# Optimization experiments

Hardware: AMD Instinct MI355X
Metric: run time of the kernel (lower is better)

The kernel has to match this reference:

```python
import jax, jax.numpy as jnp
import numpy as np

BETA = 0.25

def setup_inputs() -> dict:
    key = jax.random.key(0)
    k1, k2 = jax.random.split(key)
    x = jax.random.normal(k1, (16, 256, 32, 32), dtype=jnp.float32)
    emb_weight = jax.random.normal(k2, (8192, 256), dtype=jnp.float32) * 0.02
    return {"x": x, "emb_weight": emb_weight}

def reference(x, emb_weight):
    # b c h w -> b h w c
    xt = jnp.transpose(x, (0, 2, 3, 1))
    D = emb_weight.shape[1]
    xf = xt.reshape(-1, D)  # [N, D]
    # squared euclidean distances: [N, K]
    dist = (jnp.sum(xf * xf, axis=1, keepdims=True)
            + jnp.sum(emb_weight * emb_weight, axis=1)
            - 2.0 * xf @ emb_weight.T)
    indices = jnp.argmin(dist, axis=1)  # [N]
    x_q = emb_weight[indices].reshape(xt.shape)  # [B,H,W,D]
    sg = jax.lax.stop_gradient
    loss = (BETA * jnp.mean(jnp.square(sg(x_q) - xt))
            + jnp.mean(jnp.square(x_q - sg(xt))))
    # straight-through estimator
    x_q_st = xt + sg(x_q - xt)
    out = jnp.transpose(x_q_st, (0, 3, 1, 2))  # b h w c -> b c h w
    return out, loss, indices
```

## Files before the change

kernel.cpp:

```cpp
#include <hip/hip_runtime.h>

#define NPTS   16384
#define KCODES 8192
#define DDIM   256
#define HWSZ   1024
#define CHW    (DDIM * HWSZ)
#define OUT_ELEMS 4194304
#define LOSS_OFF  OUT_ELEMS
#define IDX_OFF   (OUT_ELEMS + 1)

#define PTB   64
#define CTILE 128
#define KC    64
#define NIT   256
#define XPITCH 264

#define ARENA_B 133120
#define XH_OFF  65536
#define XL_OFF  99328

typedef _Float16 half_t;
typedef __attribute__((ext_vector_type(8))) _Float16 half8;
typedef __attribute__((ext_vector_type(4))) float     v4f;

union HU { _Float16 h; unsigned short u; };

#define EHI_WORDS  (256 * 8192)
#define SE_OFF_B   (2 * EHI_WORDS * 2)

#define GLD16(gp, lp) __builtin_amdgcn_global_load_lds( \
    (const __attribute__((address_space(1))) unsigned int*)(gp), \
    (__attribute__((address_space(3))) unsigned int*)(lp), 16, 0, 0)

__global__ void prep_kernel(const float* __restrict__ emb,
                            unsigned short* __restrict__ ehi,
                            unsigned short* __restrict__ elo,
                            float* __restrict__ se)
{
    const int gw   = (blockIdx.x * 256 + threadIdx.x) >> 6;
    const int lane = threadIdx.x & 63;
    for (int i = 0; i < 8; ++i) {
        const int c = gw * 8 + i;
        const float4 v = *(const float4*)(emb + (size_t)c * DDIM + lane * 4);
        float ps = v.x * v.x;
        ps = fmaf(v.y, v.y, ps); ps = fmaf(v.z, v.z, ps); ps = fmaf(v.w, v.w, ps);
        float tot = ps;
        #pragma unroll
        for (int off = 1; off < 64; off <<= 1) tot += __shfl_xor(tot, off);
        if (lane == 0) se[c] = tot;
        const float E0 = v.x * 64.f, E1 = v.y * 64.f, E2 = v.z * 64.f, E3 = v.w * 64.f;
        const half_t h0 = (half_t)E0, h1 = (half_t)E1, h2 = (half_t)E2, h3 = (half_t)E3;
        const half_t l0 = (half_t)((E0 - (float)h0) * 2048.f);
        const half_t l1 = (half_t)((E1 - (float)h1) * 2048.f);
        const half_t l2 = (half_t)((E2 - (float)h2) * 2048.f);
        const half_t l3 = (half_t)((E3 - (float)h3) * 2048.f);
        HU a0, a1, a2, a3, b0, b1, b2, b3;
        a0.h = h0; a1.h = h1; a2.h = h2; a3.h = h3;
        b0.h = l0; b1.h = l1; b2.h = l2; b3.h = l3;
        const unsigned int uh0 = (unsigned)a0.u | ((unsigned)a1.u << 16);
        const unsigned int uh1 = (unsigned)a2.u | ((unsigned)a3.u << 16);
        const unsigned int ul0 = (unsigned)b0.u | ((unsigned)b1.u << 16);
        const unsigned int ul1 = (unsigned)b2.u | ((unsigned)b3.u << 16);
        const int ck = lane >> 4;
        const int kb = (lane & 15) >> 1;
        const int hf = lane & 1;
        const int T = c >> 7, r = c & 127;
        const size_t base = (((size_t)(T * 4 + ck) * 128 + r) * 64)
                          + (size_t)((kb ^ (r & 7)) * 8) + hf * 4;
        *(unsigned int*)&ehi[base]     = uh0;
        *(unsigned int*)&ehi[base + 2] = uh1;
        *(unsigned int*)&elo[base]     = ul0;
        *(unsigned int*)&elo[base + 2] = ul1;
    }
}

__launch_bounds__(512)
__global__ void vq_kernel(const float* __restrict__ x,
                          const unsigned short* __restrict__ ehi,
                          const unsigned short* __restrict__ elo,
                          const float* __restrict__ wse,
                          const float* __restrict__ emb,
                          float* __restrict__ out)
{
    __shared__ __align__(16) char ldsA[ARENA_B];
    __shared__ float  ldsRS[8][65];
    __shared__ float  ldsS[PTB];
    __shared__ float  ldsFD[8][32];
    __shared__ int    ldsFI[8][32];
    __shared__ int    ldsI[PTB];
    __shared__ double ldsL[8];

    const int t    = threadIdx.x;
    const int lane = t & 63;
    const int w    = t >> 6;
    const int n0   = blockIdx.x * PTB;
    const int b    = n0 / HWSZ;
    const int hw0  = n0 % HWSZ;
    const float* xs = x + (size_t)b * CHW + hw0;

    unsigned short* XHp = (unsigned short*)(ldsA + XH_OFF);
    unsigned short* XLp = (unsigned short*)(ldsA + XL_OFF);

    const int part = (w & 3) * 4096;
    #define STAGE(img, q) do { \
        const char* _g = (const char*)((w < 4) ? ehi : elo) \
                       + (size_t)(img) * 16384 + part + lane * 16; \
        char* _l = ldsA + (size_t)(q) * 32768 + ((w < 4) ? 0 : 16384) + part; \
        GLD16(_g,          _l); \
        GLD16(_g + 1024,   _l + 1024); \
        GLD16(_g + 2048,   _l + 2048); \
        GLD16(_g + 3072,   _l + 3072); \
    } while (0)

    STAGE(0, 0);
    STAGE(1, 1);

    {
        const int p   = t & 63;
        const int seg = t >> 6;
        float a = 0.f;
        for (int i = 0; i < 32; ++i) {
            const int c = seg * 32 + i;
            const float v = xs[(size_t)c * HWSZ + p];
            const half_t hh = (half_t)v;
            const half_t hl = (half_t)((v - (float)hh) * 2048.0f);
            HU u0; u0.h = hh; XHp[p * XPITCH + c] = u0.u;
            HU u1; u1.h = hl; XLp[p * XPITCH + c] = u1.u;
            a = fmaf(v, v, a);
        }
        ldsRS[seg][p] = a;
    }
    __syncthreads();
    if (t < PTB) {
        float s = 0.f;
        for (int g = 0; g < 8; ++g) s += ldsRS[g][t];
        ldsS[t] = s;
    }
    __syncthreads();

    const int h32 = (w & 1) * 32;
    const int q32 = (w >> 1) * 32;
    const int ln  = lane & 15;
    const int qd  = lane >> 4;

    float s_frag[8];
    #pragma unroll
    for (int pbi = 0; pbi < 2; ++pbi)
        #pragma unroll
        for (int r = 0; r < 4; ++r)
            s_frag[pbi * 4 + r] = ldsS[h32 + pbi * 16 + qd * 4 + r];

    half8 aH[2][4][2], aL[2][4][2];
    #pragma unroll
    for (int pb = 0; pb < 2; ++pb)
        #pragma unroll
        for (int ck = 0; ck < 4; ++ck)
            #pragma unroll
            for (int kk = 0; kk < 2; ++kk) {
                const int ka = ck * KC + kk * 32 + qd * 8;
                aH[pb][ck][kk] = *(const half8*)&XHp[(h32 + pb * 16 + ln) * XPITCH + ka];
                aL[pb][ck][kk] = *(const half8*)&XLp[(h32 + pb * 16 + ln) * XPITCH + ka];
            }
    asm volatile("s_waitcnt lgkmcnt(0)" ::: "memory");
    __syncthreads();

    float best_d[8]; int best_i[8];
    #pragma unroll
    for (int i = 0; i < 8; ++i) { best_d[i] = 3.4e38f; best_i[i] = 0; }

    v4f acc_hh[2][2], acc_hl[2][2];
    float se0 = 0.f, se1 = 0.f;

    const int rL = (q32 + ln) * 64;
    const int rH = (q32 + 16 + ln) * 64;

    #define CHUNK(CK) do { \
        const unsigned short* EHp = (const unsigned short*)(ldsA + (CK) * 32768); \
        const unsigned short* ELp = (const unsigned short*)(ldsA + (CK) * 32768 + 16384); \
        _Pragma("unroll") \
        for (int kk = 0; kk < 2; ++kk) { \
            const int swz = ((kk * 4 + qd) ^ (ln & 7)) * 8; \
            const half8 bh0 = *(const half8*)&EHp[rL + swz]; \
            const half8 bh1 = *(const half8*)&EHp[rH + swz]; \
            const half8 bl0 = *(const half8*)&ELp[rL + swz]; \
            const half8 bl1 = *(const half8*)&ELp[rH + swz]; \
            acc_hh[0][0] = __builtin_amdgcn_mfma_f32_16x16x32_f16(aH[0][CK][kk], bh0, acc_hh[0][0], 0, 0, 0); \
            acc_hh[0][1] = __builtin_amdgcn_mfma_f32_16x16x32_f16(aH[0][CK][kk], bh1, acc_hh[0][1], 0, 0, 0); \
            acc_hh[1][0] = __builtin_amdgcn_mfma_f32_16x16x32_f16(aH[1][CK][kk], bh0, acc_hh[1][0], 0, 0, 0); \
            acc_hh[1][1] = __builtin_amdgcn_mfma_f32_16x16x32_f16(aH[1][CK][kk], bh1, acc_hh[1][1], 0, 0, 0); \
            acc_hl[0][0] = __builtin_amdgcn_mfma_f32_16x16x32_f16(aH[0][CK][kk], bl0, acc_hl[0][0], 0, 0, 0); \
            acc_hl[0][1] = __builtin_amdgcn_mfma_f32_16x16x32_f16(aH[0][CK][kk], bl1, acc_hl[0][1], 0, 0, 0); \
            acc_hl[1][0] = __builtin_amdgcn_mfma_f32_16x16x32_f16(aH[1][CK][kk], bl0, acc_hl[1][0], 0, 0, 0); \
            acc_hl[1][1] = __builtin_amdgcn_mfma_f32_16x16x32_f16(aH[1][CK][kk], bl1, acc_hl[1][1], 0, 0, 0); \
            acc_hl[0][0] = __builtin_amdgcn_mfma_f32_16x16x32_f16(aL[0][CK][kk], bh0, acc_hl[0][0], 0, 0, 0); \
            acc_hl[0][1] = __builtin_amdgcn_mfma_f32_16x16x32_f16(aL[0][CK][kk], bh1, acc_hl[0][1], 0, 0, 0); \
            acc_hl[1][0] = __builtin_amdgcn_mfma_f32_16x16x32_f16(aL[1][CK][kk], bh0, acc_hl[1][0], 0, 0, 0); \
            acc_hl[1][1] = __builtin_amdgcn_mfma_f32_16x16x32_f16(aL[1][CK][kk], bh1, acc_hl[1][1], 0, 0, 0); \
        } \
    } while (0)

    for (int tile = 0; tile < 64; ++tile) {
        const int it0 = tile * 4;
        __builtin_amdgcn_s_barrier();
        STAGE(it0 + 2, 2);
        STAGE(it0 + 3, 3);
        asm volatile("s_waitcnt vmcnt(8)" ::: "memory");
        __builtin_amdgcn_s_barrier();
        __builtin_amdgcn_s_setprio(1);
        #pragma unroll
        for (int i = 0; i < 2; ++i)
            #pragma unroll
            for (int j = 0; j < 2; ++j)
                #pragma unroll
                for (int r = 0; r < 4; ++r) { acc_hh[i][j][r] = 0.f; acc_hl[i][j][r] = 0.f; }
        CHUNK(0);
        CHUNK(1);
        __builtin_amdgcn_s_setprio(0);
        {
            const int tb2 = tile * CTILE;
            se0 = wse[tb2 + q32 + ln];
            se1 = wse[tb2 + q32 + 16 + ln];
        }
        __builtin_amdgcn_s_barrier();
        if (tile + 1 < 64) {
            STAGE(it0 + 4, 0);
            STAGE(it0 + 5, 1);
            asm volatile("s_waitcnt vmcnt(8)" ::: "memory");
        } else {
            asm volatile("s_waitcnt vmcnt(0)" ::: "memory");
        }
        __builtin_amdgcn_s_barrier();
        __builtin_amdgcn_s_setprio(1);
        CHUNK(2);
        CHUNK(3);
        __builtin_amdgcn_s_setprio(0);
        {
            const int tb = tile * CTILE;
            #pragma unroll
            for (int csi = 0; csi < 2; ++csi) {
                const float se   = csi ? se1 : se0;
                const int   code = tb + q32 + csi * 16 + ln;
                #pragma unroll
                for (int pbi = 0; pbi < 2; ++pbi)
                    #pragma unroll
                    for (int r = 0; r < 4; ++r) {
                        const float m  = fmaf(acc_hl[pbi][csi][r], 4.8828125e-4f,
                                              acc_hh[pbi][csi][r]) * 0.015625f;
                        const float T  = s_frag[pbi * 4 + r] + se;
                        const float dd = fmaf(-2.0f, m, T);
                        const int   s  = pbi * 4 + r;
                        if (dd < best_d[s]) { best_d[s] = dd; best_i[s] = code; }
                    }
            }
        }
    }

    #pragma unroll
    for (int off = 1; off < 16; off <<= 1) {
        #pragma unroll
        for (int s = 0; s < 8; ++s) {
            const float d2 = __shfl_xor(best_d[s], off);
            const int   i2 = __shfl_xor(best_i[s], off);
            if (d2 < best_d[s] || (d2 == best_d[s] && i2 < best_i[s])) {
                best_d[s] = d2; best_i[s] = i2;
            }
        }
    }
    if (ln == 0) {
        #pragma unroll
        for (int pbi = 0; pbi < 2; ++pbi)
            #pragma unroll
            for (int r = 0; r < 4; ++r) {
                ldsFD[w][pbi * 16 + qd * 4 + r] = best_d[pbi * 4 + r];
                ldsFI[w][pbi * 16 + qd * 4 + r] = best_i[pbi * 4 + r];
            }
    }
    __syncthreads();
    if (t < PTB) {
        const int hh  = t >> 5;
        const int r32 = t & 31;
        float bd = 3.4e38f; int bi = 0;
        #pragma unroll
        for (int qq = 0; qq < 4; ++qq) {
            const int wv = hh + qq * 2;
            const float d2 = ldsFD[wv][r32];
            const int   i2 = ldsFI[wv][r32];
            if (d2 < bd || (d2 == bd && i2 < bi)) { bd = d2; bi = i2; }
        }
        ldsI[t] = bi;
        out[(size_t)IDX_OFF + n0 + t] = (float)bi;
    }
    __syncthreads();

    double lsum = 0.0;
    {
        const int p  = t & 63;
        const int cg = t >> 6;
        const int row = ldsI[p];
        const float* erow = emb + (size_t)row * DDIM;
        float* ob = out + (size_t)b * CHW + hw0 + p;
        for (int q = 0; q < 32; ++q) {
            const int c = cg * 32 + q;
            const float e  = erow[c];
            const float xx = xs[(size_t)c * HWSZ + p];
            const float diff = e - xx;
            ob[(size_t)c * HWSZ] = xx + diff;
            lsum += (double)diff * (double)diff;
        }
    }
    #pragma unroll
    for (int off = 32; off > 0; off >>= 1)
        lsum += __shfl_xor(lsum, off);
    if ((t & 63) == 0) ldsL[t >> 6] = lsum;
    __syncthreads();
    if (t == 0) {
        double tot = 0.0;
        #pragma unroll
        for (int wv = 0; wv < 8; ++wv) tot += ldsL[wv];
        atomicAdd(&out[LOSS_OFF], (float)(tot * (1.25 / 4194304.0)));
    }
}

extern "C" void kernel_launch(void* const* d_in, const int* in_sizes, int n_in,
                              void* d_out, int out_size, void* d_ws, size_t ws_size,
                              hipStream_t stream) {
    (void)in_sizes; (void)n_in; (void)out_size; (void)ws_size;
    const float* x   = (const float*)d_in[0];
    const float* emb = (const float*)d_in[1];
    float* out = (float*)d_out;
    unsigned short* ehi = (unsigned short*)d_ws;
    unsigned short* elo = ehi + EHI_WORDS;
    float*          wse = (float*)((char*)d_ws + SE_OFF_B);
    hipMemsetAsync((char*)d_out + (size_t)LOSS_OFF * sizeof(float), 0, sizeof(float), stream);
    prep_kernel<<<256, 256, 0, stream>>>(emb, ehi, elo, wse);
    vq_kernel<<<NPTS / PTB, 512, 0, stream>>>(x, ehi, elo, wse, emb, out);
}
```

Baseline: 310.2 us.

## Halve points per block and use double-buffered codebook staging to raise occupancy

Blocks now process 32 points with 4 waves instead of 64 points with 8 waves. The LDS arena shrinks from about 130KB to 64KB by overlaying the X staging area onto the codebook buffers. The 4-deep prefetch with manual waitcnt and priority tricks becomes a simple 2-stage double buffer with a __syncthreads per chunk. The goal is more resident blocks per CU and better latency hiding. In exchange, each block reloads the entire codebook for half as many points, doubling global and LDS traffic per point, and pays more barriers.

```diff
diff --git a/kernel.cpp b/kernel.cpp
--- a/kernel.cpp
+++ b/kernel.cpp
@@ -9,15 +9,15 @@
 #define LOSS_OFF  OUT_ELEMS
 #define IDX_OFF   (OUT_ELEMS + 1)
 
-#define PTB   64
+#define PTB   32
 #define CTILE 128
 #define KC    64
 #define NIT   256
 #define XPITCH 264
 
-#define ARENA_B 133120
-#define XH_OFF  65536
-#define XL_OFF  99328
+#define ARENA_B 65536
+#define XH_OFF  0
+#define XL_OFF  16896
 
 typedef _Float16 half_t;
 typedef __attribute__((ext_vector_type(8))) _Float16 half8;
@@ -74,7 +74,7 @@
     }
 }
 
-__launch_bounds__(512)
+__launch_bounds__(256)
 __global__ void vq_kernel(const float* __restrict__ x,
                           const unsigned short* __restrict__ ehi,
                           const unsigned short* __restrict__ elo,
@@ -83,12 +83,12 @@
                           float* __restrict__ out)
 {
     __shared__ __align__(16) char ldsA[ARENA_B];
-    __shared__ float  ldsRS[8][65];
+    __shared__ float  ldsRS[8][33];
     __shared__ float  ldsS[PTB];
-    __shared__ float  ldsFD[8][32];
-    __shared__ int    ldsFI[8][32];
+    __shared__ float  ldsFD[4][32];
+    __shared__ int    ldsFI[4][32];
     __shared__ int    ldsI[PTB];
-    __shared__ double ldsL[8];
+    __shared__ double ldsL[4];
 
     const int t    = threadIdx.x;
     const int lane = t & 63;
@@ -101,23 +101,24 @@
     unsigned short* XHp = (unsigned short*)(ldsA + XH_OFF);
     unsigned short* XLp = (unsigned short*)(ldsA + XL_OFF);
 
-    const int part = (w & 3) * 4096;
+    const int part = (w & 1) * 8192;
     #define STAGE(img, q) do { \
-        const char* _g = (const char*)((w < 4) ? ehi : elo) \
+        const char* _g = (const char*)((w < 2) ? ehi : elo) \
                        + (size_t)(img) * 16384 + part + lane * 16; \
-        char* _l = ldsA + (size_t)(q) * 32768 + ((w < 4) ? 0 : 16384) + part; \
+        char* _l = ldsA + (size_t)(q) * 32768 + ((w < 2) ? 0 : 16384) + part; \
         GLD16(_g,          _l); \
         GLD16(_g + 1024,   _l + 1024); \
         GLD16(_g + 2048,   _l + 2048); \
         GLD16(_g + 3072,   _l + 3072); \
+        GLD16(_g + 4096,   _l + 4096); \
+        GLD16(_g + 5120,   _l + 5120); \
+        GLD16(_g + 6144,   _l + 6144); \
+        GLD16(_g + 7168,   _l + 7168); \
     } while (0)
 
-    STAGE(0, 0);
-    STAGE(1, 1);
-
     {
-        const int p   = t & 63;
-        const int seg = t >> 6;
+        const int p   = t & 31;
+        const int seg = t >> 5;
         float a = 0.f;
         for (int i = 0; i < 32; ++i) {
             const int c = seg * 32 + i;
@@ -138,8 +139,7 @@
     }
     __syncthreads();
 
-    const int h32 = (w & 1) * 32;
-    const int q32 = (w >> 1) * 32;
+    const int q32 = w * 32;
     const int ln  = lane & 15;
     const int qd  = lane >> 4;
 
@@ -148,7 +148,7 @@
     for (int pbi = 0; pbi < 2; ++pbi)
         #pragma unroll
         for (int r = 0; r < 4; ++r)
-            s_frag[pbi * 4 + r] = ldsS[h32 + pbi * 16 + qd * 4 + r];
+            s_frag[pbi * 4 + r] = ldsS[pbi * 16 + qd * 4 + r];
 
     half8 aH[2][4][2], aL[2][4][2];
     #pragma unroll
@@ -158,11 +158,12 @@
             #pragma unroll
             for (int kk = 0; kk < 2; ++kk) {
                 const int ka = ck * KC + kk * 32 + qd * 8;
-                aH[pb][ck][kk] = *(const half8*)&XHp[(h32 + pb * 16 + ln) * XPITCH + ka];
-                aL[pb][ck][kk] = *(const half8*)&XLp[(h32 + pb * 16 + ln) * XPITCH + ka];
-            }
-    asm volatile("s_waitcnt lgkmcnt(0)" ::: "memory");
-    __syncthreads();
+                aH[pb][ck][kk] = *(const half8*)&XHp[(pb * 16 + ln) * XPITCH + ka];
+                aL[pb][ck][kk] = *(const half8*)&XLp[(pb * 16 + ln) * XPITCH + ka];
+            }
+    __syncthreads();
+
+    STAGE(0, 0);
 
     float best_d[8]; int best_i[8];
     #pragma unroll
@@ -175,8 +176,8 @@
     const int rH = (q32 + 16 + ln) * 64;
 
     #define CHUNK(CK) do { \
-        const unsigned short* EHp = (const unsigned short*)(ldsA + (CK) * 32768); \
-        const unsigned short* ELp = (const unsigned short*)(ldsA + (CK) * 32768 + 16384); \
+        const unsigned short* EHp = (const unsigned short*)(ldsA + ((CK) & 1) * 32768); \
+        const unsigned short* ELp = (const unsigned short*)(ldsA + ((CK) & 1) * 32768 + 16384); \
         _Pragma("unroll") \
         for (int kk = 0; kk < 2; ++kk) { \
             const int swz = ((kk * 4 + qd) ^ (ln & 7)) * 8; \
@@ -200,57 +201,41 @@
     } while (0)
 
     for (int tile = 0; tile < 64; ++tile) {
-        const int it0 = tile * 4;
-        __builtin_amdgcn_s_barrier();
-        STAGE(it0 + 2, 2);
-        STAGE(it0 + 3, 3);
-        asm volatile("s_waitcnt vmcnt(8)" ::: "memory");
-        __builtin_amdgcn_s_barrier();
-        __builtin_amdgcn_s_setprio(1);
         #pragma unroll
         for (int i = 0; i < 2; ++i)
             #pragma unroll
             for (int j = 0; j < 2; ++j)
                 #pragma unroll
                 for (int r = 0; r < 4; ++r) { acc_hh[i][j][r] = 0.f; acc_hl[i][j][r] = 0.f; }
-        CHUNK(0);
-        CHUNK(1);
-        __builtin_amdgcn_s_setprio(0);
-        {
-            const int tb2 = tile * CTILE;
-            se0 = wse[tb2 + q32 + ln];
-            se1 = wse[tb2 + q32 + 16 + ln];
-        }
-        __builtin_amdgcn_s_barrier();
-        if (tile + 1 < 64) {
-            STAGE(it0 + 4, 0);
-            STAGE(it0 + 5, 1);
-            asm volatile("s_waitcnt vmcnt(8)" ::: "memory");
-        } else {
-            asm volatile("s_waitcnt vmcnt(0)" ::: "memory");
-        }
-        __builtin_amdgcn_s_barrier();
-        __builtin_amdgcn_s_setprio(1);
-        CHUNK(2);
-        CHUNK(3);
-        __builtin_amdgcn_s_setprio(0);
-        {
-            const int tb = tile * CTILE;
-            #pragma unroll
-            for (int csi = 0; csi < 2; ++csi) {
-                const float se   = csi ? se1 : se0;
-                const int   code = tb + q32 + csi * 16 + ln;
+        #pragma unroll
+        for (int ck = 0; ck < 4; ++ck) {
+            const int it = tile * 4 + ck;
+            __syncthreads();
+            if (it + 1 < NIT) STAGE(it + 1, (ck + 1) & 1);
+            if (ck == 2) {
+                const int tb2 = tile * CTILE;
+                se0 = wse[tb2 + q32 + ln];
+                se1 = wse[tb2 + q32 + 16 + ln];
+            }
+            CHUNK(ck);
+            if (ck == 3) {
+                const int tb = tile * CTILE;
                 #pragma unroll
-                for (int pbi = 0; pbi < 2; ++pbi)
+                for (int csi = 0; csi < 2; ++csi) {
+                    const float se   = csi ? se1 : se0;
+                    const int   code = tb + q32 + csi * 16 + ln;
                     #pragma unroll
-                    for (int r = 0; r < 4; ++r) {
-                        const float m  = fmaf(acc_hl[pbi][csi][r], 4.8828125e-4f,
-                                              acc_hh[pbi][csi][r]) * 0.015625f;
-                        const float T  = s_frag[pbi * 4 + r] + se;
-                        const float dd = fmaf(-2.0f, m, T);
-                        const int   s  = pbi * 4 + r;
-                        if (dd < best_d[s]) { best_d[s] = dd; best_i[s] = code; }
-                    }
+                    for (int pbi = 0; pbi < 2; ++pbi)
+                        #pragma unroll
+                        for (int r = 0; r < 4; ++r) {
+                            const float m  = fmaf(acc_hl[pbi][csi][r], 4.8828125e-4f,
+                                                  acc_hh[pbi][csi][r]) * 0.015625f;
+                            const float T  = s_frag[pbi * 4 + r] + se;
+                            const float dd = fmaf(-2.0f, m, T);
+                            const int   s  = pbi * 4 + r;
+                            if (dd < best_d[s]) { best_d[s] = dd; best_i[s] = code; }
+                        }
+                }
             }
         }
     }
@@ -277,14 +262,11 @@
     }
     __syncthreads();
     if (t < PTB) {
-        const int hh  = t >> 5;
-        const int r32 = t & 31;
         float bd = 3.4e38f; int bi = 0;
         #pragma unroll
         for (int qq = 0; qq < 4; ++qq) {
-            const int wv = hh + qq * 2;
-            const float d2 = ldsFD[wv][r32];
-            const int   i2 = ldsFI[wv][r32];
+            const float d2 = ldsFD[qq][t];
+            const int   i2 = ldsFI[qq][t];
             if (d2 < bd || (d2 == bd && i2 < bi)) { bd = d2; bi = i2; }
         }
         ldsI[t] = bi;
@@ -294,8 +276,8 @@
 
     double lsum = 0.0;
     {
-        const int p  = t & 63;
-        const int cg = t >> 6;
+        const int p  = t & 31;
+        const int cg = t >> 5;
         const int row = ldsI[p];
         const float* erow = emb + (size_t)row * DDIM;
         float* ob = out + (size_t)b * CHW + hw0 + p;
@@ -316,7 +298,7 @@
     if (t == 0) {
         double tot = 0.0;
         #pragma unroll
-        for (int wv = 0; wv < 8; ++wv) tot += ldsL[wv];
+        for (int wv = 0; wv < 4; ++wv) tot += ldsL[wv];
         atomicAdd(&out[LOSS_OFF], (float)(tot * (1.25 / 4194304.0)));
     }
 }
@@ -333,5 +315,5 @@
     float*          wse = (float*)((char*)d_ws + SE_OFF_B);
     hipMemsetAsync((char*)d_out + (size_t)LOSS_OFF * sizeof(float), 0, sizeof(float), stream);
     prep_kernel<<<256, 256, 0, stream>>>(emb, ehi, elo, wse);
-    vq_kernel<<<NPTS / PTB, 512, 0, stream>>>(x, ehi, elo, wse, emb, out);
+    vq_kernel<<<NPTS / PTB, 256, 0, stream>>>(x, ehi, elo, wse, emb, out);
 }
```

Result: slower. 495.0 us (+59.6%).

## Prefetch codebook fragments into registers with two LDS staging buffers

Applied to the files above, without the earlier changes.

Splits the single shared-memory arena into named X and codebook buffers and cuts codebook staging from four LDS chunks to two. Each chunk's B fragments are now read into registers (bA/bB) one chunk ahead, so the MFMAs of chunk N run while chunk N+1 is read from LDS and chunk N+2 is fetched from global memory. The goal is to hide LDS read latency behind the matrix ops. In exchange, the global prefetch distance drops and a full __syncthreads (which also waits for outstanding memory ops) sits between every chunk, which may expose global load latency.

```diff
diff --git a/kernel.cpp b/kernel.cpp
--- a/kernel.cpp
+++ b/kernel.cpp
@@ -14,10 +14,6 @@
 #define KC    64
 #define NIT   256
 #define XPITCH 264
-
-#define ARENA_B 133120
-#define XH_OFF  65536
-#define XL_OFF  99328
 
 typedef _Float16 half_t;
 typedef __attribute__((ext_vector_type(8))) _Float16 half8;
@@ -82,7 +78,10 @@
                           const float* __restrict__ emb,
                           float* __restrict__ out)
 {
-    __shared__ __align__(16) char ldsA[ARENA_B];
+    __shared__ __align__(16) unsigned short ldsXH[PTB][XPITCH];
+    __shared__ __align__(16) unsigned short ldsXL[PTB][XPITCH];
+    __shared__ __align__(16) unsigned short ldsEH[2][8192];
+    __shared__ __align__(16) unsigned short ldsEL[2][8192];
     __shared__ float  ldsRS[8][65];
     __shared__ float  ldsS[PTB];
     __shared__ float  ldsFD[8][32];
@@ -98,14 +97,11 @@
     const int hw0  = n0 % HWSZ;
     const float* xs = x + (size_t)b * CHW + hw0;
 
-    unsigned short* XHp = (unsigned short*)(ldsA + XH_OFF);
-    unsigned short* XLp = (unsigned short*)(ldsA + XL_OFF);
-
     const int part = (w & 3) * 4096;
-    #define STAGE(img, q) do { \
+    #define STAGE(img, buf) do { \
         const char* _g = (const char*)((w < 4) ? ehi : elo) \
                        + (size_t)(img) * 16384 + part + lane * 16; \
-        char* _l = ldsA + (size_t)(q) * 32768 + ((w < 4) ? 0 : 16384) + part; \
+        char* _l = (char*)((w < 4) ? ldsEH[buf] : ldsEL[buf]) + part; \
         GLD16(_g,          _l); \
         GLD16(_g + 1024,   _l + 1024); \
         GLD16(_g + 2048,   _l + 2048); \
@@ -113,7 +109,6 @@
     } while (0)
 
     STAGE(0, 0);
-    STAGE(1, 1);
 
     {
         const int p   = t & 63;
@@ -124,8 +119,8 @@
             const float v = xs[(size_t)c * HWSZ + p];
             const half_t hh = (half_t)v;
             const half_t hl = (half_t)((v - (float)hh) * 2048.0f);
-            HU u0; u0.h = hh; XHp[p * XPITCH + c] = u0.u;
-            HU u1; u1.h = hl; XLp[p * XPITCH + c] = u1.u;
+            HU u0; u0.h = hh; ldsXH[p][c] = u0.u;
+            HU u1; u1.h = hl; ldsXL[p][c] = u1.u;
             a = fmaf(v, v, a);
         }
         ldsRS[seg][p] = a;
@@ -158,11 +153,9 @@
             #pragma unroll
             for (int kk = 0; kk < 2; ++kk) {
                 const int ka = ck * KC + kk * 32 + qd * 8;
-                aH[pb][ck][kk] = *(const half8*)&XHp[(h32 + pb * 16 + ln) * XPITCH + ka];
-                aL[pb][ck][kk] = *(const half8*)&XLp[(h32 + pb * 16 + ln) * XPITCH + ka];
+                aH[pb][ck][kk] = *(const half8*)&ldsXH[h32 + pb * 16 + ln][ka];
+                aL[pb][ck][kk] = *(const half8*)&ldsXL[h32 + pb * 16 + ln][ka];
             }
-    asm volatile("s_waitcnt lgkmcnt(0)" ::: "memory");
-    __syncthreads();
 
     float best_d[8]; int best_i[8];
     #pragma unroll
@@ -174,16 +167,24 @@
     const int rL = (q32 + ln) * 64;
     const int rH = (q32 + 16 + ln) * 64;
 
-    #define CHUNK(CK) do { \
-        const unsigned short* EHp = (const unsigned short*)(ldsA + (CK) * 32768); \
-        const unsigned short* ELp = (const unsigned short*)(ldsA + (CK) * 32768 + 16384); \
+    half8 bA[8], bB[8];
+
+    #define READF(SET, BUF) do { \
         _Pragma("unroll") \
         for (int kk = 0; kk < 2; ++kk) { \
             const int swz = ((kk * 4 + qd) ^ (ln & 7)) * 8; \
-            const half8 bh0 = *(const half8*)&EHp[rL + swz]; \
-            const half8 bh1 = *(const half8*)&EHp[rH + swz]; \
-            const half8 bl0 = *(const half8*)&ELp[rL + swz]; \
-            const half8 bl1 = *(const half8*)&ELp[rH + swz]; \
+            SET[kk * 4 + 0] = *(const half8*)&ldsEH[BUF][rL + swz]; \
+            SET[kk * 4 + 1] = *(const half8*)&ldsEH[BUF][rH + swz]; \
+            SET[kk * 4 + 2] = *(const half8*)&ldsEL[BUF][rL + swz]; \
+            SET[kk * 4 + 3] = *(const half8*)&ldsEL[BUF][rH + swz]; \
+        } \
+    } while (0)
+
+    #define MFMAC(SET, CK) do { \
+        _Pragma("unroll") \
+        for (int kk = 0; kk < 2; ++kk) { \
+            const half8 bh0 = SET[kk * 4 + 0], bh1 = SET[kk * 4 + 1]; \
+            const half8 bl0 = SET[kk * 4 + 2], bl1 = SET[kk * 4 + 3]; \
             acc_hh[0][0] = __builtin_amdgcn_mfma_f32_16x16x32_f16(aH[0][CK][kk], bh0, acc_hh[0][0], 0, 0, 0); \
             acc_hh[0][1] = __builtin_amdgcn_mfma_f32_16x16x32_f16(aH[0][CK][kk], bh1, acc_hh[0][1], 0, 0, 0); \
             acc_hh[1][0] = __builtin_amdgcn_mfma_f32_16x16x32_f16(aH[1][CK][kk], bh0, acc_hh[1][0], 0, 0, 0); \
@@ -199,41 +200,41 @@
         } \
     } while (0)
 
+    READF(bA, 0);
+    STAGE(1, 1);
+
     for (int tile = 0; tile < 64; ++tile) {
         const int it0 = tile * 4;
-        __builtin_amdgcn_s_barrier();
-        STAGE(it0 + 2, 2);
-        STAGE(it0 + 3, 3);
-        asm volatile("s_waitcnt vmcnt(8)" ::: "memory");
-        __builtin_amdgcn_s_barrier();
-        __builtin_amdgcn_s_setprio(1);
+        __syncthreads();
+        READF(bB, 1);
+        STAGE(it0 + 2, 0);
+        __builtin_amdgcn_sched_barrier(0);
         #pragma unroll
         for (int i = 0; i < 2; ++i)
             #pragma unroll
             for (int j = 0; j < 2; ++j)
                 #pragma unroll
                 for (int r = 0; r < 4; ++r) { acc_hh[i][j][r] = 0.f; acc_hl[i][j][r] = 0.f; }
-        CHUNK(0);
-        CHUNK(1);
-        __builtin_amdgcn_s_setprio(0);
-        {
-            const int tb2 = tile * CTILE;
-            se0 = wse[tb2 + q32 + ln];
-            se1 = wse[tb2 + q32 + 16 + ln];
-        }
-        __builtin_amdgcn_s_barrier();
-        if (tile + 1 < 64) {
-            STAGE(it0 + 4, 0);
+        MFMAC(bA, 0);
+        __syncthreads();
+        READF(bA, 0);
+        STAGE(it0 + 3, 1);
+        __builtin_amdgcn_sched_barrier(0);
+        MFMAC(bB, 1);
+        __syncthreads();
+        READF(bB, 1);
+        if (tile < 63) STAGE(it0 + 4, 0);
+        se0 = wse[tile * CTILE + q32 + ln];
+        se1 = wse[tile * CTILE + q32 + 16 + ln];
+        __builtin_amdgcn_sched_barrier(0);
+        MFMAC(bA, 2);
+        __syncthreads();
+        if (tile < 63) {
+            READF(bA, 0);
             STAGE(it0 + 5, 1);
-            asm volatile("s_waitcnt vmcnt(8)" ::: "memory");
-        } else {
-            asm volatile("s_waitcnt vmcnt(0)" ::: "memory");
-        }
-        __builtin_amdgcn_s_barrier();
-        __builtin_amdgcn_s_setprio(1);
-        CHUNK(2);
-        CHUNK(3);
-        __builtin_amdgcn_s_setprio(0);
+        }
+        __builtin_amdgcn_sched_barrier(0);
+        MFMAC(bB, 3);
         {
             const int tb = tile * CTILE;
             #pragma unroll
```

Measured after the change: 386.1 us. 1.24x slower.

## Interleave half-chunk codebook staging with MFMA phases and overlap X with stage buffers

Applied to the files above, without the earlier changes.

Restructures the main loop into eight fine-grained phases. Each phase reads B fragments from LDS, issues half of the next-next chunk's global-to-LDS load, waits on vmcnt, then runs 12 MFMAs between barriers. This gives steadier load/compute overlap than the previous two big staging points. The X hi/lo staging area is now aliased onto the codebook ring buffer, shrinking the LDS arena, and the initial codebook prefetch is moved after X fragments are loaded into registers. The cost is twice as many barriers per tile and tighter vmcnt accounting.

```diff
diff --git a/kernel.cpp b/kernel.cpp
--- a/kernel.cpp
+++ b/kernel.cpp
@@ -15,9 +15,9 @@
 #define NIT   256
 #define XPITCH 264
 
-#define ARENA_B 133120
-#define XH_OFF  65536
-#define XL_OFF  99328
+#define ARENA_B 131072
+#define XH_OFF  0
+#define XL_OFF  33792
 
 typedef _Float16 half_t;
 typedef __attribute__((ext_vector_type(8))) _Float16 half8;
@@ -102,18 +102,13 @@
     unsigned short* XLp = (unsigned short*)(ldsA + XL_OFF);
 
     const int part = (w & 3) * 4096;
-    #define STAGE(img, q) do { \
+    #define STAGE_HALF(img, q, hf) do { \
         const char* _g = (const char*)((w < 4) ? ehi : elo) \
-                       + (size_t)(img) * 16384 + part + lane * 16; \
-        char* _l = ldsA + (size_t)(q) * 32768 + ((w < 4) ? 0 : 16384) + part; \
+                       + (size_t)(img) * 16384 + part + (hf) * 2048 + lane * 16; \
+        char* _l = ldsA + (size_t)(q) * 32768 + ((w < 4) ? 0 : 16384) + part + (hf) * 2048; \
         GLD16(_g,          _l); \
         GLD16(_g + 1024,   _l + 1024); \
-        GLD16(_g + 2048,   _l + 2048); \
-        GLD16(_g + 3072,   _l + 3072); \
     } while (0)
-
-    STAGE(0, 0);
-    STAGE(1, 1);
 
     {
         const int p   = t & 63;
@@ -161,8 +156,12 @@
                 aH[pb][ck][kk] = *(const half8*)&XHp[(h32 + pb * 16 + ln) * XPITCH + ka];
                 aL[pb][ck][kk] = *(const half8*)&XLp[(h32 + pb * 16 + ln) * XPITCH + ka];
             }
-    asm volatile("s_waitcnt lgkmcnt(0)" ::: "memory");
-    __syncthreads();
+    __syncthreads();
+
+    STAGE_HALF(0, 0, 0); STAGE_HALF(0, 0, 1);
+    STAGE_HALF(1, 1, 0); STAGE_HALF(1, 1, 1);
+    asm volatile("s_waitcnt vmcnt(4)" ::: "memory");
+    __builtin_amdgcn_s_barrier();
 
     float best_d[8]; int best_i[8];
     #pragma unroll
@@ -174,66 +173,60 @@
     const int rL = (q32 + ln) * 64;
     const int rH = (q32 + 16 + ln) * 64;
 
-    #define CHUNK(CK) do { \
-        const unsigned short* EHp = (const unsigned short*)(ldsA + (CK) * 32768); \
-        const unsigned short* ELp = (const unsigned short*)(ldsA + (CK) * 32768 + 16384); \
-        _Pragma("unroll") \
-        for (int kk = 0; kk < 2; ++kk) { \
-            const int swz = ((kk * 4 + qd) ^ (ln & 7)) * 8; \
-            const half8 bh0 = *(const half8*)&EHp[rL + swz]; \
-            const half8 bh1 = *(const half8*)&EHp[rH + swz]; \
-            const half8 bl0 = *(const half8*)&ELp[rL + swz]; \
-            const half8 bl1 = *(const half8*)&ELp[rH + swz]; \
-            acc_hh[0][0] = __builtin_amdgcn_mfma_f32_16x16x32_f16(aH[0][CK][kk], bh0, acc_hh[0][0], 0, 0, 0); \
-            acc_hh[0][1] = __builtin_amdgcn_mfma_f32_16x16x32_f16(aH[0][CK][kk], bh1, acc_hh[0][1], 0, 0, 0); \
-            acc_hh[1][0] = __builtin_amdgcn_mfma_f32_16x16x32_f16(aH[1][CK][kk], bh0, acc_hh[1][0], 0, 0, 0); \
-            acc_hh[1][1] = __builtin_amdgcn_mfma_f32_16x16x32_f16(aH[1][CK][kk], bh1, acc_hh[1][1], 0, 0, 0); \
-            acc_hl[0][0] = __builtin_amdgcn_mfma_f32_16x16x32_f16(aH[0][CK][kk], bl0, acc_hl[0][0], 0, 0, 0); \
-            acc_hl[0][1] = __builtin_amdgcn_mfma_f32_16x16x32_f16(aH[0][CK][kk], bl1, acc_hl[0][1], 0, 0, 0); \
-            acc_hl[1][0] = __builtin_amdgcn_mfma_f32_16x16x32_f16(aH[1][CK][kk], bl0, acc_hl[1][0], 0, 0, 0); \
-            acc_hl[1][1] = __builtin_amdgcn_mfma_f32_16x16x32_f16(aH[1][CK][kk], bl1, acc_hl[1][1], 0, 0, 0); \
-            acc_hl[0][0] = __builtin_amdgcn_mfma_f32_16x16x32_f16(aL[0][CK][kk], bh0, acc_hl[0][0], 0, 0, 0); \
-            acc_hl[0][1] = __builtin_amdgcn_mfma_f32_16x16x32_f16(aL[0][CK][kk], bh1, acc_hl[0][1], 0, 0, 0); \
-            acc_hl[1][0] = __builtin_amdgcn_mfma_f32_16x16x32_f16(aL[1][CK][kk], bh0, acc_hl[1][0], 0, 0, 0); \
-            acc_hl[1][1] = __builtin_amdgcn_mfma_f32_16x16x32_f16(aL[1][CK][kk], bh1, acc_hl[1][1], 0, 0, 0); \
+    #define MFMA12(CK, KK, BH0, BH1, BL0, BL1) do { \
+        acc_hh[0][0] = __builtin_amdgcn_mfma_f32_16x16x32_f16(aH[0][CK][KK], BH0, acc_hh[0][0], 0, 0, 0); \
+        acc_hh[0][1] = __builtin_amdgcn_mfma_f32_16x16x32_f16(aH[0][CK][KK], BH1, acc_hh[0][1], 0, 0, 0); \
+        acc_hh[1][0] = __builtin_amdgcn_mfma_f32_16x16x32_f16(aH[1][CK][KK], BH0, acc_hh[1][0], 0, 0, 0); \
+        acc_hh[1][1] = __builtin_amdgcn_mfma_f32_16x16x32_f16(aH[1][CK][KK], BH1, acc_hh[1][1], 0, 0, 0); \
+        acc_hl[0][0] = __builtin_amdgcn_mfma_f32_16x16x32_f16(aH[0][CK][KK], BL0, acc_hl[0][0], 0, 0, 0); \
+        acc_hl[0][1] = __builtin_amdgcn_mfma_f32_16x16x32_f16(aH[0][CK][KK], BL1, acc_hl[0][1], 0, 0, 0); \
+        acc_hl[1][0] = __builtin_amdgcn_mfma_f32_16x16x32_f16(aH[1][CK][KK], BL0, acc_hl[1][0], 0, 0, 0); \
+        acc_hl[1][1] = __builtin_amdgcn_mfma_f32_16x16x32_f16(aH[1][CK][KK], BL1, acc_hl[1][1], 0, 0, 0); \
+        acc_hl[0][0] = __builtin_amdgcn_mfma_f32_16x16x32_f16(aL[0][CK][KK], BH0, acc_hl[0][0], 0, 0, 0); \
+        acc_hl[0][1] = __builtin_amdgcn_mfma_f32_16x16x32_f16(aL[0][CK][KK], BH1, acc_hl[0][1], 0, 0, 0); \
+        acc_hl[1][0] = __builtin_amdgcn_mfma_f32_16x16x32_f16(aL[1][CK][KK], BH0, acc_hl[1][0], 0, 0, 0); \
+        acc_hl[1][1] = __builtin_amdgcn_mfma_f32_16x16x32_f16(aL[1][CK][KK], BH1, acc_hl[1][1], 0, 0, 0); \
+    } while (0)
+
+    #define PHASE(CK, KK) do { \
+        const unsigned short* EHp_ = (const unsigned short*)(ldsA + (CK) * 32768); \
+        const unsigned short* ELp_ = EHp_ + 8192; \
+        const int swz_ = (((KK) * 4 + qd) ^ (ln & 7)) * 8; \
+        const half8 bh0_ = *(const half8*)&EHp_[rL + swz_]; \
+        const half8 bh1_ = *(const half8*)&EHp_[rH + swz_]; \
+        const half8 bl0_ = *(const half8*)&ELp_[rL + swz_]; \
+        const half8 bl1_ = *(const half8*)&ELp_[rH + swz_]; \
+        const int it_ = it0 + (CK); \
+        if (it_ + 2 < NIT) STAGE_HALF(it_ + 2, ((CK) + 2) & 3, KK); \
+        if ((KK) == 1) { \
+            if (it_ + 2 < NIT)      { asm volatile("s_waitcnt vmcnt(4)" ::: "memory"); } \
+            else if (it_ + 1 < NIT) { asm volatile("s_waitcnt vmcnt(0)" ::: "memory"); } \
+            if ((CK) == 2) { \
+                se0 = wse[tile * CTILE + q32 + ln]; \
+                se1 = wse[tile * CTILE + q32 + 16 + ln]; \
+            } \
         } \
+        __builtin_amdgcn_s_barrier(); \
+        __builtin_amdgcn_s_setprio(1); \
+        MFMA12(CK, KK, bh0_, bh1_, bl0_, bl1_); \
+        __builtin_amdgcn_s_setprio(0); \
+        __builtin_amdgcn_s_barrier(); \
     } while (0)
 
     for (int tile = 0; tile < 64; ++tile) {
         const int it0 = tile * 4;
-        __builtin_amdgcn_s_barrier();
-        STAGE(it0 + 2, 2);
-        STAGE(it0 + 3, 3);
-        asm volatile("s_waitcnt vmcnt(8)" ::: "memory");
-        __builtin_amdgcn_s_barrier();
-        __builtin_amdgcn_s_setprio(1);
         #pragma unroll
         for (int i = 0; i < 2; ++i)
             #pragma unroll
             for (int j = 0; j < 2; ++j)
                 #pragma unroll
                 for (int r = 0; r < 4; ++r) { acc_hh[i][j][r] = 0.f; acc_hl[i][j][r] = 0.f; }
-        CHUNK(0);
-        CHUNK(1);
-        __builtin_amdgcn_s_setprio(0);
-        {
-            const int tb2 = tile * CTILE;
-            se0 = wse[tb2 + q32 + ln];
-            se1 = wse[tb2 + q32 + 16 + ln];
-        }
-        __builtin_amdgcn_s_barrier();
-        if (tile + 1 < 64) {
-            STAGE(it0 + 4, 0);
-            STAGE(it0 + 5, 1);
-            asm volatile("s_waitcnt vmcnt(8)" ::: "memory");
-        } else {
-            asm volatile("s_waitcnt vmcnt(0)" ::: "memory");
-        }
-        __builtin_amdgcn_s_barrier();
-        __builtin_amdgcn_s_setprio(1);
-        CHUNK(2);
-        CHUNK(3);
-        __builtin_amdgcn_s_setprio(0);
+
+        PHASE(0, 0); PHASE(0, 1);
+        PHASE(1, 0); PHASE(1, 1);
+        PHASE(2, 0); PHASE(2, 1);
+        PHASE(3, 0); PHASE(3, 1);
+
         {
             const int tb = tile * CTILE;
             #pragma unroll
```

New measurement: 278.6 us. 10.2% less time.
